# Performance work log

Measured on AMD Instinct MI355X. Metric: run time of the kernel, lower is better.

## Reference

```python
import jax, jax.numpy as jnp
import numpy as np

CONF_THRES = 0.7
IOU_THRES = 0.45
TOP_K = 1000  # max candidates kept per image after confidence filtering (YOLOv5 max_nms-style cap)
IMG_SIZE = 640.0


def _box_iou(boxes):
    """Pairwise IoU of [K,4] xyxy boxes -> [K,K]."""
    area = (boxes[:, 2] - boxes[:, 0]) * (boxes[:, 3] - boxes[:, 1])
    lt = jnp.maximum(boxes[:, None, :2], boxes[None, :, :2])
    rb = jnp.minimum(boxes[:, None, 2:], boxes[None, :, 2:])
    wh = jnp.clip(rb - lt, 0.0)
    inter = wh[..., 0] * wh[..., 1]
    return inter / (area[:, None] + area[None, :] - inter + 1e-7)


def _nms_single(pred):
    """YOLOv5-style NMS for one image. pred: [N, 9] = xywh, obj, cls_conf, pitch, yaw, roll.
    Returns fixed-shape padded detections [TOP_K, 9] and keep mask [TOP_K]."""
    obj = pred[:, 4]
    conf = obj * pred[:, 5]  # nc=1: conf = obj_conf * cls_conf
    valid = (obj > CONF_THRES) & (conf > CONF_THRES)
    score = jnp.where(valid, conf, -1.0)

    top_scores, idx = jax.lax.top_k(score, TOP_K)
    p = pred[idx]  # [TOP_K, 9]
    xy, wh = p[:, :2], p[:, 2:4]
    boxes = jnp.concatenate([xy - wh * 0.5, xy + wh * 0.5], axis=-1)  # xywh -> xyxy

    keep0 = top_scores > CONF_THRES
    iou = _box_iou(boxes)  # [TOP_K, TOP_K]
    ar = jnp.arange(TOP_K)

    # Greedy NMS: boxes are score-sorted; box j is suppressed if a kept earlier box overlaps > thresh.
    def body(i, keep):
        sup = (iou[i] > IOU_THRES) & (ar > i) & keep[i]
        return keep & (~sup)

    keep = jax.lax.fori_loop(0, TOP_K, body, keep0)

    cls = jnp.zeros((TOP_K, 1), boxes.dtype)  # single class (head)
    out = jnp.concatenate([boxes, top_scores[:, None], cls, p[:, 6:9]], axis=-1)  # [TOP_K, 9]
    out = out * keep[:, None].astype(out.dtype)  # zero padded/suppressed rows
    return out, keep


def setup_inputs() -> dict:
    key = jax.random.key(0)
    B, N = 32, 25200
    r = jax.random.uniform(key, (B, N, 9), dtype=jnp.float32)
    xy = r[..., :2] * IMG_SIZE                 # box centers in pixels
    wh = r[..., 2:4] * 128.0 + 4.0             # box sizes 4..132 px
    obj = r[..., 4:5]                          # objectness in [0,1)
    cls = r[..., 5:6] * 0.5 + 0.5              # class conf in [0.5,1)
    ang = (r[..., 6:9] - 0.5) * 2.0            # normalized pitch/yaw/roll
    prediction = jnp.concatenate([xy, wh, obj, cls, ang], axis=-1)
    return {"prediction": prediction}


def reference(prediction):
    out, keep = jax.vmap(_nms_single)(prediction)
    return out, keep
```

## Files before the change

### kernel.cpp

```cpp
#include <hip/hip_runtime.h>
#include <stdint.h>

#pragma clang fp contract(off)

#define BATCH 32
#define NPRED 25200
#define ROWF 9
#define TOPK 1000
#define SUBS 8
#define ROWS_PER_SUB (NPRED / SUBS)
#define SUBCAP 512
#define CONF_T 0.7f
#define IOU_T 0.45f
#define KW 16
#define SUPROW 1024
#define TKROW 1024

typedef unsigned long long u64;
typedef unsigned int u32;

#define WS_CAND 0
#define WS_BX   (1048576)
#define WS_SA   (WS_BX + 524288)
#define WS_SUP  (WS_SA + 524288)


__device__ __forceinline__ u64 readlane64(u64 v, int l) {
    u32 lo = __builtin_amdgcn_readlane((u32)v, (u32)l);
    u32 hi = __builtin_amdgcn_readlane((u32)(v >> 32), (u32)l);
    return ((u64)hi << 32) | lo;
}
__device__ __forceinline__ float readlanef(float v, int l) {
    return __uint_as_float(__builtin_amdgcn_readlane(__float_as_uint(v), (u32)l));
}
__device__ __forceinline__ u64 shflxor64(u64 v, int m) {
    u32 lo = __shfl_xor((u32)v, m, 64);
    u32 hi = __shfl_xor((u32)(v >> 32), m, 64);
    return ((u64)hi << 32) | lo;
}

__global__ __launch_bounds__(512) void compact_sort_kernel(const float* __restrict__ pred,
                                                           u64* __restrict__ cand_ws,
                                                           float4* __restrict__ bx_ws,
                                                           float4* __restrict__ sa_ws) {
    __shared__ u64 skey[SUBCAP];
    __shared__ u32 cnt;
    int bs = blockIdx.x;
    int b = bs >> 3, s = bs & 7;
    int tid = threadIdx.x;
    if (tid == 0) cnt = 0;
    skey[tid] = 0;
    if (tid < 128) {
        float4 z = make_float4(0.f, 0.f, 0.f, 0.f);
        bx_ws[(size_t)b * TKROW + s * 128 + tid] = z;
        sa_ws[(size_t)b * TKROW + s * 128 + tid] = z;
    }
    __syncthreads();

    int r0 = s * ROWS_PER_SUB;
    const int NCH = (ROWS_PER_SUB + 511) / 512;
    float objv[NCH], clsv[NCH];
#pragma unroll
    for (int k = 0; k < NCH; ++k) {
        int r = tid + k * 512;
        if (r < ROWS_PER_SUB) {
            size_t base = ((size_t)b * NPRED + r0 + r) * ROWF;
            objv[k] = pred[base + 4];
            clsv[k] = pred[base + 5];
        }
    }
#pragma unroll
    for (int k = 0; k < NCH; ++k) {
        int r = tid + k * 512;
        if (r < ROWS_PER_SUB) {
            float conf = objv[k] * clsv[k];
            if (objv[k] > CONF_T && conf > CONF_T) {
                int row = r0 + r;
                u32 slot = atomicAdd(&cnt, 1u);
                if (slot < SUBCAP)
                    skey[slot] = ((u64)__float_as_uint(conf) << 32) | (u64)(u32)(~(u32)row);
            }
        }
    }
    __syncthreads();

    u64 key = skey[tid];
    bool wrote = true;
    for (int k = 2; k <= SUBCAP; k <<= 1) {
        for (int j = k >> 1; j > 0; j >>= 1) {
            bool desc = ((tid & k) == 0);
            bool up = ((tid & j) == 0);
            u64 part;
            if (j >= 64) {
                if (!wrote) { __syncthreads(); skey[tid] = key; }
                __syncthreads();
                part = skey[tid ^ j];
                wrote = false;
            } else {
                part = shflxor64(key, j);
                wrote = false;
            }
            bool takemax = (desc == up);
            u64 mx = key > part ? key : part;
            u64 mn = key > part ? part : key;
            key = takemax ? mx : mn;
        }
    }
    cand_ws[(size_t)bs * SUBCAP + tid] = key;
}

__global__ __launch_bounds__(512) void rank_kernel(const float* __restrict__ pred,
                                                   const u64* __restrict__ cand_ws,
                                                   float4* __restrict__ bx_ws,
                                                   float4* __restrict__ sa_ws) {
    __shared__ u64 lists[SUBS * SUBCAP];
    int bs = blockIdx.x;
    int b = bs >> 3, s = bs & 7;
    int tid = threadIdx.x;
    const u64* src = cand_ws + (size_t)b * SUBS * SUBCAP;
    for (int t = tid; t < SUBS * SUBCAP; t += 512) lists[t] = src[t];
    __syncthreads();
    u64 key = lists[(s << 9) + tid];
    if (key) {
        int lo[SUBS];
#pragma unroll
        for (int l = 0; l < SUBS; ++l) lo[l] = 0;
#pragma unroll
        for (int w2 = SUBCAP; w2 >= 1; w2 >>= 1) {
#pragma unroll
            for (int l = 0; l < SUBS; ++l) {
                int p = lo[l] + w2;
                if (p <= SUBCAP && lists[(l << 9) + p - 1] > key) lo[l] = p;
            }
        }
        int rank = 0;
#pragma unroll
        for (int l = 0; l < SUBS; ++l) rank += lo[l];
        if (rank < TOPK) {
            u32 r = ~(u32)key;
            const float* p = pred + ((size_t)b * NPRED + r) * ROWF;
            float x = p[0], y = p[1], wd = p[2], hh = p[3];
            float4 box = make_float4(x - wd * 0.5f, y - hh * 0.5f,
                                     x + wd * 0.5f, y + hh * 0.5f);
            float4 sa = make_float4(__uint_as_float((u32)(key >> 32)),
                                    p[6], p[7], p[8]);
            bx_ws[(size_t)b * TKROW + rank] = box;
            sa_ws[(size_t)b * TKROW + rank] = sa;
        }
    }
}

__global__ __launch_bounds__(1024) void supmat_kernel(const float4* __restrict__ bx_ws,
                                                      u64* __restrict__ sup_g) {
    __shared__ float4 bx_s[1024];
    __shared__ float  ar_s[1024];
    int b = blockIdx.x >> 3, q = blockIdx.x & 7;
    int tid = threadIdx.x;
    {
        float4 box = bx_ws[(size_t)b * TKROW + tid];
        bx_s[tid] = box;
        ar_s[tid] = (box.z - box.x) * (box.w - box.y);
    }
    __syncthreads();
    int wave = tid >> 6, lane = tid & 63;
    for (int pass = 0; pass < 2; ++pass) {
        int t = (pass == 0) ? (q * 16 + wave) : ((wave == 15) ? 128 + q : 136);
        if (t >= 136) continue;
        int iw = 0, rem = t, c = 16;
        while (rem >= c) { rem -= c; c--; iw++; }
        int jw = iw + rem;
        int i = iw * 64 + lane;
        bool act = i < TOPK;
        float4 bi4 = bx_s[i];
        float ai = ar_s[i];
        float4 bja = bx_s[(jw << 6) + lane];
        float aja = ar_s[(jw << 6) + lane];
        u64 m = 0;
        int jbase = jw << 6;
        for (int l2 = 0; l2 < 64; ++l2) {
            float bjx = readlanef(bja.x, l2);
            float bjy = readlanef(bja.y, l2);
            float bjz = readlanef(bja.z, l2);
            float bjw = readlanef(bja.w, l2);
            float aj  = readlanef(aja, l2);
            float lx = fmaxf(bi4.x, bjx);
            float ly = fmaxf(bi4.y, bjy);
            float rx = fminf(bi4.z, bjz);
            float ry = fminf(bi4.w, bjw);
            float iw2 = rx - lx; iw2 = iw2 > 0.f ? iw2 : 0.f;
            float ih = ry - ly; ih = ih > 0.f ? ih : 0.f;
            float inter = iw2 * ih;
            float den = ai + aj - inter + 1e-7f;
            float iou = inter / den;
            if (act && (jbase + l2) > i && iou > IOU_T) m |= 1ull << l2;
        }
        if (act) sup_g[((size_t)b * KW + jw) * SUPROW + i] = m;
    }
}

__global__ __launch_bounds__(1024) void scan_out_kernel(const float4* __restrict__ bx_ws,
                                                        const float4* __restrict__ sa_ws,
                                                        const u64* __restrict__ sup_g,
                                                        float* __restrict__ out,
                                                        float* __restrict__ keepout) {
    __shared__ u64 keep_lds[KW];
    __shared__ u64 acc_lds;
    int b = blockIdx.x, tid = threadIdx.x;
    int w = tid >> 6, lane = tid & 63;
    const u64* S = sup_g + (size_t)b * KW * SUPROW;

    float4 sa = sa_ws[(size_t)b * TKROW + tid];
    u64 keep0 = __ballot(sa.x != 0.f);
    if (lane == 0) keep_lds[w] = keep0;

    u64 sup_reg[KW];
    u64 diagreg = 0;
#pragma unroll
    for (int bi = 0; bi < KW; ++bi) {
        sup_reg[bi] = 0;
        if (bi <= w)
            sup_reg[bi] = S[(size_t)w * SUPROW + (bi << 6) + lane];
        if (bi == w) diagreg = sup_reg[bi];
    }
    __syncthreads();

    u64 nzmask = __ballot(diagreg != 0);

#pragma unroll
    for (int bi = 0; bi < KW; ++bi) {
        if (w == bi) {
            u64 cur = keep_lds[bi];
            u64 active = cur & nzmask;
            while (active) {
                int i = __ffsll((long long)active) - 1;
                u64 wi = readlane64(diagreg, i);
                active &= active - 1;
                cur &= ~wi;
                active &= ~wi;
            }
            if (lane == 0) { keep_lds[bi] = cur; acc_lds = cur; }
        }
        __syncthreads();
        if (w > bi) {
            u64 A = acc_lds;
            u64 myv = sup_reg[bi];
            bool accb = (A >> lane) & 1ull;
            u64 lanes = __ballot(accb && myv != 0ull);
            if (lanes) {
                u64 wred = 0;
                while (lanes) {
                    int l = __ffsll((long long)lanes) - 1;
                    wred |= readlane64(myv, l);
                    lanes &= lanes - 1;
                }
                if (lane == 0) keep_lds[w] &= ~wred;
            }
        }
        __syncthreads();
    }

    if (tid < TOPK) {
        bool kp = ((keep_lds[w] >> lane) & 1ull) != 0;
        float4 bx = bx_ws[(size_t)b * TKROW + tid];
        size_t ob = ((size_t)b * TOPK + tid) * ROWF;
        out[ob + 0] = kp ? bx.x : 0.f;
        out[ob + 1] = kp ? bx.y : 0.f;
        out[ob + 2] = kp ? bx.z : 0.f;
        out[ob + 3] = kp ? bx.w : 0.f;
        out[ob + 4] = kp ? sa.x : 0.f;
        out[ob + 5] = 0.f;
        out[ob + 6] = kp ? sa.y : 0.f;
        out[ob + 7] = kp ? sa.z : 0.f;
        out[ob + 8] = kp ? sa.w : 0.f;
        keepout[(size_t)b * TOPK + tid] = kp ? 1.0f : 0.0f;
    }
}

extern "C" void kernel_launch(void* const* d_in, const int* in_sizes, int n_in,
                              void* d_out, int out_size, void* d_ws, size_t ws_size,
                              hipStream_t stream) {
    const float* pred = (const float*)d_in[0];
    float* out = (float*)d_out;
    float* keepout = out + (size_t)BATCH * TOPK * ROWF;
    char* ws = (char*)d_ws;
    u64* cand_ws = (u64*)(ws + WS_CAND);
    float4* bx_ws = (float4*)(ws + WS_BX);
    float4* sa_ws = (float4*)(ws + WS_SA);
    u64* sup_g = (u64*)(ws + WS_SUP);

    compact_sort_kernel<<<BATCH * SUBS, 512, 0, stream>>>(pred, cand_ws, bx_ws, sa_ws);
    rank_kernel<<<BATCH * SUBS, 512, 0, stream>>>(pred, cand_ws, bx_ws, sa_ws);
    supmat_kernel<<<BATCH * SUBS, 1024, 0, stream>>>(bx_ws, sup_g);
    scan_out_kernel<<<BATCH, 1024, 0, stream>>>(bx_ws, sa_ws, sup_g, out, keepout);
}
```

Before: 123.6 us.

## Fuse suppression-matrix and greedy scan kernels via last-block atomic counter

Merges the supmat and scan_out kernels into one launch. Each of the 8 blocks per image builds its slice of the suppression bitmask, then bumps a per-image atomic counter, and the last block to arrive runs the greedy scan and writes the output. The counters are reset in the first kernel. This removes one kernel launch and its boundary, and reuses the boxes already staged in LDS, at the cost of a threadfence plus atomic and a scan tail that runs only in the last block per image.

```diff
diff --git a/kernel.cpp b/kernel.cpp
--- a/kernel.cpp
+++ b/kernel.cpp
@@ -23,6 +23,7 @@
 #define WS_BX   (1048576)
 #define WS_SA   (WS_BX + 524288)
 #define WS_SUP  (WS_SA + 524288)
+#define WS_FLAGS (WS_SUP + 4194304)
 
 
 __device__ __forceinline__ u64 readlane64(u64 v, int l) {
@@ -42,7 +43,8 @@
 __global__ __launch_bounds__(512) void compact_sort_kernel(const float* __restrict__ pred,
                                                            u64* __restrict__ cand_ws,
                                                            float4* __restrict__ bx_ws,
-                                                           float4* __restrict__ sa_ws) {
+                                                           float4* __restrict__ sa_ws,
+                                                           u32* __restrict__ flags) {
     __shared__ u64 skey[SUBCAP];
     __shared__ u32 cnt;
     int bs = blockIdx.x;
@@ -55,6 +57,7 @@
         bx_ws[(size_t)b * TKROW + s * 128 + tid] = z;
         sa_ws[(size_t)b * TKROW + s * 128 + tid] = z;
     }
+    if (tid == 0 && bs < BATCH) flags[bs] = 0;
     __syncthreads();
 
     int r0 = s * ROWS_PER_SUB;
@@ -150,21 +153,29 @@
     }
 }
 
-__global__ __launch_bounds__(1024) void supmat_kernel(const float4* __restrict__ bx_ws,
-                                                      u64* __restrict__ sup_g) {
+__global__ __launch_bounds__(1024) void supscan_kernel(const float4* __restrict__ bx_ws,
+                                                       const float4* __restrict__ sa_ws,
+                                                       u64* __restrict__ sup_g,
+                                                       u32* __restrict__ flags,
+                                                       float* __restrict__ out,
+                                                       float* __restrict__ keepout) {
     __shared__ float4 bx_s[1024];
     __shared__ float  ar_s[1024];
+    __shared__ u64 keep_lds[KW];
+    __shared__ u64 acc_lds;
+    __shared__ u32 last_sh;
     int b = blockIdx.x >> 3, q = blockIdx.x & 7;
     int tid = threadIdx.x;
+    int w = tid >> 6, lane = tid & 63;
+
     {
         float4 box = bx_ws[(size_t)b * TKROW + tid];
         bx_s[tid] = box;
         ar_s[tid] = (box.z - box.x) * (box.w - box.y);
     }
     __syncthreads();
-    int wave = tid >> 6, lane = tid & 63;
     for (int pass = 0; pass < 2; ++pass) {
-        int t = (pass == 0) ? (q * 16 + wave) : ((wave == 15) ? 128 + q : 136);
+        int t = (pass == 0) ? (q * 16 + w) : ((w == 15) ? 128 + q : 136);
         if (t >= 136) continue;
         int iw = 0, rem = t, c = 16;
         while (rem >= c) { rem -= c; c--; iw++; }
@@ -196,19 +207,16 @@
         }
         if (act) sup_g[((size_t)b * KW + jw) * SUPROW + i] = m;
     }
-}
-
-__global__ __launch_bounds__(1024) void scan_out_kernel(const float4* __restrict__ bx_ws,
-                                                        const float4* __restrict__ sa_ws,
-                                                        const u64* __restrict__ sup_g,
-                                                        float* __restrict__ out,
-                                                        float* __restrict__ keepout) {
-    __shared__ u64 keep_lds[KW];
-    __shared__ u64 acc_lds;
-    int b = blockIdx.x, tid = threadIdx.x;
-    int w = tid >> 6, lane = tid & 63;
+
+    __threadfence();
+    __syncthreads();
+    if (tid == 0)
+        last_sh = __hip_atomic_fetch_add(&flags[b], 1u, __ATOMIC_ACQ_REL,
+                                         __HIP_MEMORY_SCOPE_AGENT);
+    __syncthreads();
+    if (last_sh != 7u) return;
+
     const u64* S = sup_g + (size_t)b * KW * SUPROW;
-
     float4 sa = sa_ws[(size_t)b * TKROW + tid];
     u64 keep0 = __ballot(sa.x != 0.f);
     if (lane == 0) keep_lds[w] = keep0;
@@ -261,7 +269,7 @@
 
     if (tid < TOPK) {
         bool kp = ((keep_lds[w] >> lane) & 1ull) != 0;
-        float4 bx = bx_ws[(size_t)b * TKROW + tid];
+        float4 bx = bx_s[tid];
         size_t ob = ((size_t)b * TOPK + tid) * ROWF;
         out[ob + 0] = kp ? bx.x : 0.f;
         out[ob + 1] = kp ? bx.y : 0.f;
@@ -287,9 +295,9 @@
     float4* bx_ws = (float4*)(ws + WS_BX);
     float4* sa_ws = (float4*)(ws + WS_SA);
     u64* sup_g = (u64*)(ws + WS_SUP);
-
-    compact_sort_kernel<<<BATCH * SUBS, 512, 0, stream>>>(pred, cand_ws, bx_ws, sa_ws);
+    u32* flags = (u32*)(ws + WS_FLAGS);
+
+    compact_sort_kernel<<<BATCH * SUBS, 512, 0, stream>>>(pred, cand_ws, bx_ws, sa_ws, flags);
     rank_kernel<<<BATCH * SUBS, 512, 0, stream>>>(pred, cand_ws, bx_ws, sa_ws);
-    supmat_kernel<<<BATCH * SUBS, 1024, 0, stream>>>(bx_ws, sup_g);
-    scan_out_kernel<<<BATCH, 1024, 0, stream>>>(bx_ws, sa_ws, sup_g, out, keepout);
-}
+    supscan_kernel<<<BATCH * SUBS, 1024, 0, stream>>>(bx_ws, sa_ws, sup_g, flags, out, keepout);
+}
```

Result: slower. 176.3 us (+42.7%).
